# Optimization experiments

Measured on AMD Instinct MI355X. Metric: run time of the kernel, lower is better.

The kernel has to match this reference:

```python
import jax, jax.numpy as jnp
import numpy as np

B, INDIM, OUTDIM = 1024, 2048, 4096


def setup_inputs() -> dict:
    key = jax.random.key(0)
    kx, kw, kb = jax.random.split(key, 3)
    x = jax.random.normal(kx, (B, INDIM), dtype=jnp.float32)
    # nn.Linear(indim, outdim): weight [outdim, indim], bias [outdim]
    bound = 1.0 / np.sqrt(INDIM)
    W = jax.random.uniform(kw, (OUTDIM, INDIM), minval=-bound, maxval=bound, dtype=jnp.float32)
    b = jax.random.uniform(kb, (OUTDIM,), minval=-bound, maxval=bound, dtype=jnp.float32)
    return {"x": x, "W": W, "b": b}


def reference(x, W, b):
    # Faithful to torch: prototypes = weight.transpose(0,1).reshape(outdim, indim)
    # (a reflatten of W^T, not the original weight rows, since outdim != indim).
    protos = W.T.reshape(W.shape[0], W.shape[1])  # [outdim, indim]
    # -||x_i - p_j||^2 - b_j via GEMM identity (same math as broadcast subtract + norm^2)
    x_sq = jnp.sum(x * x, axis=1, keepdims=True)          # [B, 1]
    p_sq = jnp.sum(protos * protos, axis=1)[None, :]      # [1, outdim]
    xp = jnp.einsum('bd,od->bo', x, protos)               # [B, outdim]
    return -(x_sq - 2.0 * xp + p_sq) - b[None, :]
```

## Files before the change

### kernel.cpp

```cpp
#include <hip/hip_runtime.h>

#define IN_DIM  2048
#define OUT_DIM 4096

typedef float     f32x4 __attribute__((ext_vector_type(4)));
typedef long long llx2  __attribute__((ext_vector_type(2)));

__device__ __forceinline__ unsigned int pk4(float a, float b, float c, float d) {
    int v = __builtin_amdgcn_cvt_pk_fp8_f32(a, b, 0, false);
    v     = __builtin_amdgcn_cvt_pk_fp8_f32(c, d, v, true);
    return (unsigned int)v;
}

__device__ __forceinline__ void async16(const void* g, void* l) {
    __builtin_amdgcn_global_load_lds(
        (const __attribute__((address_space(1))) unsigned int*)g,
        (__attribute__((address_space(3))) unsigned int*)l,
        16, 0, 0);
}

__device__ __forceinline__ int gmem_of(int c) { return 2 * (c & 3) + (c >> 2); }

extern "C" __global__ __launch_bounds__(256) void prep(
        const float* __restrict__ W, const float* __restrict__ x,
        unsigned char* __restrict__ protos, unsigned char* __restrict__ xb,
        float* __restrict__ psq_part, float* __restrict__ x_sq) {
    __shared__ float tile[64][65];
    const int t = threadIdx.x;

    if (blockIdx.z == 2) {
        const int b = blockIdx.x + 32 * blockIdx.y;
        const float* xp = x + (size_t)b * IN_DIM + t * 8;
        const float4 v0 = ((const float4*)xp)[0];
        const float4 v1 = ((const float4*)xp)[1];
        uint2 pk;
        pk.x = pk4(v0.x, v0.y, v0.z, v0.w);
        pk.y = pk4(v1.x, v1.y, v1.z, v1.w);
        *(uint2*)(xb + (size_t)b * IN_DIM + (t >> 3) * 64 + gmem_of(t & 7) * 8) = pk;

        float s = v0.x * v0.x + v0.y * v0.y + v0.z * v0.z + v0.w * v0.w
                + v1.x * v1.x + v1.y * v1.y + v1.z * v1.z + v1.w * v1.w;
#pragma unroll
        for (int off = 32; off > 0; off >>= 1) s += __shfl_down(s, off);
        const int lane = t & 63, w = t >> 6;
        if (lane == 0) tile[0][w] = s;
        __syncthreads();
        if (t == 0) x_sq[b] = tile[0][0] + tile[0][1] + tile[0][2] + tile[0][3];
        return;
    }

    const int r  = blockIdx.z;
    const int c0 = blockIdx.x * 64;
    const int d0 = blockIdx.y * 64;
    const int g  = t >> 4;
    const int cc = (t & 15) * 4;

    const float* Wp = W + (size_t)(r * IN_DIM + d0 + g) * IN_DIM + c0 + cc;
#pragma unroll
    for (int p = 0; p < 4; ++p) {
        const float4 v = *(const float4*)(Wp + (size_t)(16 * p) * IN_DIM);
        const int dl = g + 16 * p;
        tile[dl][cc]     = v.x;
        tile[dl][cc + 1] = v.y;
        tile[dl][cc + 2] = v.z;
        tile[dl][cc + 3] = v.w;
    }
    __syncthreads();

    const int c8 = t & 7;
    const int gm = gmem_of(c8);
#pragma unroll
    for (int p = 0; p < 2; ++p) {
        const int cr = (t >> 3) + 32 * p;
        float v[8];
        float ss = 0.f;
#pragma unroll
        for (int j = 0; j < 8; ++j) {
            v[j] = tile[8 * c8 + j][cr];
            ss += v[j] * v[j];
        }
        const int o = 2 * (c0 + cr) + r;
        uint2 pk;
        pk.x = pk4(16.f * v[0], 16.f * v[1], 16.f * v[2], 16.f * v[3]);
        pk.y = pk4(16.f * v[4], 16.f * v[5], 16.f * v[6], 16.f * v[7]);
        *(uint2*)(protos + (size_t)o * IN_DIM + d0 + gm * 8) = pk;
        ss += __shfl_xor(ss, 1);
        ss += __shfl_xor(ss, 2);
        ss += __shfl_xor(ss, 4);
        if (c8 == 0) psq_part[(size_t)blockIdx.y * OUT_DIM + o] = ss;
    }
}

extern "C" __global__ __launch_bounds__(256, 4) void gemm_epi(
        const unsigned char* __restrict__ A,
        const unsigned char* __restrict__ Bt,
        const float* __restrict__ x_sq,
        const float* __restrict__ psq_part,
        const float* __restrict__ bias,
        float* __restrict__ out) {
    __shared__ __align__(16) unsigned char smem[16384];
    unsigned char* lA = smem;

    const int lid = blockIdx.x;
    const int xcd = lid & 7;
    const int wi  = lid >> 3;
    const int nt  = xcd * 8 + (wi & 7);
    const int mt  = wi >> 3;
    const int m0 = mt * 64;
    const int n0 = nt * 64;

    const int t = threadIdx.x;
    const int rS = t >> 3;
    const int pS = t & 7;
    const int lS = pS ^ (rS & 7);
    const size_t goff = (size_t)(lS >> 2) * 1024 + (lS & 3) * 16;
    const unsigned char* gA0 = A  + (size_t)(m0 + rS) * IN_DIM + goff;
    const unsigned char* gA1 = gA0 + (size_t)32 * IN_DIM;
    unsigned char* lAd = lA + t * 16;

    const int wave = t >> 6;
    const int lane = t & 63;
    const int kh = wave & 1;
    const int nh = wave >> 1;
    const int ln = lane & 15;
    const int qd = lane >> 4;
    const int pr = (kh * 4 + qd) ^ (ln & 7);

    const unsigned char* gBf = Bt + (size_t)(n0 + nh * 32 + ln) * IN_DIM
                                  + kh * 1024 + qd * 16;

    f32x4 acc[4][2] = {};

    for (int it = 0; it < 16; ++it) {
        async16(gA0, lAd); async16(gA1, lAd + 4096);
        gA0 += 64; gA1 += 64;
        llx2 bf[2];
        bf[0] = *(const llx2*)(gBf);
        bf[1] = *(const llx2*)(gBf + (size_t)16 * IN_DIM);
        gBf += 64;
        __syncthreads();

        llx2 af[4];
#pragma unroll
        for (int i = 0; i < 4; ++i)
            af[i] = *(const llx2*)(lA + (i * 16 + ln) * 128 + pr * 16);
#pragma unroll
        for (int kk = 0; kk < 2; ++kk)
#pragma unroll
            for (int i = 0; i < 4; ++i)
#pragma unroll
                for (int j = 0; j < 2; ++j)
                    acc[i][j] = __builtin_amdgcn_mfma_f32_16x16x32_fp8_fp8(
                                    af[i][kk], bf[j][kk], acc[i][j], 0, 0, 0);
        __syncthreads();
    }

    if (kh == 1) {
#pragma unroll
        for (int i = 0; i < 4; ++i)
#pragma unroll
            for (int j = 0; j < 2; ++j)
                *(f32x4*)(smem + nh * 8192 + (i * 2 + j) * 1024 + lane * 16) =
                    acc[i][j];
    }
    __syncthreads();
    if (kh == 0) {
#pragma unroll
        for (int j = 0; j < 2; ++j) {
            const int col = n0 + nh * 32 + j * 16 + ln;
            float pb = bias[col];
#pragma unroll
            for (int dt = 0; dt < 32; ++dt)
                pb += psq_part[(size_t)dt * OUT_DIM + col];
#pragma unroll
            for (int i = 0; i < 4; ++i) {
                const f32x4 o4 = *(const f32x4*)(smem + nh * 8192 +
                                                 (i * 2 + j) * 1024 + lane * 16);
                const int row0 = m0 + i * 16 + qd * 4;
#pragma unroll
                for (int rr = 0; rr < 4; ++rr) {
                    const int row = row0 + rr;
                    out[(size_t)row * OUT_DIM + col] =
                        0.125f * (acc[i][j][rr] + o4[rr]) - x_sq[row] - pb;
                }
            }
        }
    }
}

extern "C" void kernel_launch(void* const* d_in, const int* in_sizes, int n_in,
                              void* d_out, int out_size, void* d_ws, size_t ws_size,
                              hipStream_t stream) {
    const float* x    = (const float*)d_in[0];
    const float* W    = (const float*)d_in[1];
    const float* bias = (const float*)d_in[2];
    float* out = (float*)d_out;

    char* ws = (char*)d_ws;
    unsigned char* protos = (unsigned char*)ws;
    unsigned char* xb     = (unsigned char*)(ws + (size_t)8 * 1024 * 1024);
    float* x_sq           = (float*)(ws + (size_t)10 * 1024 * 1024);
    float* psq_part       = (float*)(ws + (size_t)10 * 1024 * 1024 + 65536);

    prep<<<dim3(32, 32, 3), 256, 0, stream>>>(W, x, protos, xb, psq_part, x_sq);
    gemm_epi<<<dim3(1024), 256, 0, stream>>>(xb, protos, x_sq, psq_part, bias, out);
}
```

Baseline: 115.2 us.

## Drop LDS staging and split-K; load GEMM operands directly from global memory

Removes the LDS staging of A tiles and the split-K across wave pairs. Each wave now reads its A and B fragments straight from global memory, with 64x128 tiles per block and 512 blocks, and there is no shared-memory reduction or barrier. This removes synchronization and the cross-wave reduction in the epilogue. In exchange, all four waves redundantly load the same A rows from global and cache, and the loop has a longer serial K. Memory latency is also no longer hidden by async LDS loads.

```diff
diff --git a/kernel.cpp b/kernel.cpp
--- a/kernel.cpp
+++ b/kernel.cpp
@@ -10,13 +10,6 @@
     int v = __builtin_amdgcn_cvt_pk_fp8_f32(a, b, 0, false);
     v     = __builtin_amdgcn_cvt_pk_fp8_f32(c, d, v, true);
     return (unsigned int)v;
-}
-
-__device__ __forceinline__ void async16(const void* g, void* l) {
-    __builtin_amdgcn_global_load_lds(
-        (const __attribute__((address_space(1))) unsigned int*)g,
-        (__attribute__((address_space(3))) unsigned int*)l,
-        16, 0, 0);
 }
 
 __device__ __forceinline__ int gmem_of(int c) { return 2 * (c & 3) + (c >> 2); }
@@ -91,59 +84,40 @@
     }
 }
 
-extern "C" __global__ __launch_bounds__(256, 4) void gemm_epi(
+extern "C" __global__ __launch_bounds__(256) void gemm_epi(
         const unsigned char* __restrict__ A,
         const unsigned char* __restrict__ Bt,
         const float* __restrict__ x_sq,
         const float* __restrict__ psq_part,
         const float* __restrict__ bias,
         float* __restrict__ out) {
-    __shared__ __align__(16) unsigned char smem[16384];
-    unsigned char* lA = smem;
-
     const int lid = blockIdx.x;
     const int xcd = lid & 7;
     const int wi  = lid >> 3;
-    const int nt  = xcd * 8 + (wi & 7);
-    const int mt  = wi >> 3;
+    const int nt  = xcd * 4 + (wi & 3);
+    const int mt  = wi >> 2;
     const int m0 = mt * 64;
-    const int n0 = nt * 64;
+    const int n0 = nt * 128;
 
     const int t = threadIdx.x;
-    const int rS = t >> 3;
-    const int pS = t & 7;
-    const int lS = pS ^ (rS & 7);
-    const size_t goff = (size_t)(lS >> 2) * 1024 + (lS & 3) * 16;
-    const unsigned char* gA0 = A  + (size_t)(m0 + rS) * IN_DIM + goff;
-    const unsigned char* gA1 = gA0 + (size_t)32 * IN_DIM;
-    unsigned char* lAd = lA + t * 16;
-
     const int wave = t >> 6;
     const int lane = t & 63;
-    const int kh = wave & 1;
-    const int nh = wave >> 1;
     const int ln = lane & 15;
     const int qd = lane >> 4;
-    const int pr = (kh * 4 + qd) ^ (ln & 7);
 
-    const unsigned char* gBf = Bt + (size_t)(n0 + nh * 32 + ln) * IN_DIM
-                                  + kh * 1024 + qd * 16;
+    const unsigned char* gA = A  + (size_t)(m0 + ln) * IN_DIM + qd * 16;
+    const unsigned char* gB = Bt + (size_t)(n0 + wave * 32 + ln) * IN_DIM + qd * 16;
 
     f32x4 acc[4][2] = {};
 
-    for (int it = 0; it < 16; ++it) {
-        async16(gA0, lAd); async16(gA1, lAd + 4096);
-        gA0 += 64; gA1 += 64;
-        llx2 bf[2];
-        bf[0] = *(const llx2*)(gBf);
-        bf[1] = *(const llx2*)(gBf + (size_t)16 * IN_DIM);
-        gBf += 64;
-        __syncthreads();
-
-        llx2 af[4];
+    for (int it = 0; it < 32; ++it) {
+        llx2 af[4], bf[2];
 #pragma unroll
         for (int i = 0; i < 4; ++i)
-            af[i] = *(const llx2*)(lA + (i * 16 + ln) * 128 + pr * 16);
+            af[i] = *(const llx2*)(gA + (size_t)(i * 16) * IN_DIM + it * 64);
+#pragma unroll
+        for (int j = 0; j < 2; ++j)
+            bf[j] = *(const llx2*)(gB + (size_t)(j * 16) * IN_DIM + it * 64);
 #pragma unroll
         for (int kk = 0; kk < 2; ++kk)
 #pragma unroll
@@ -152,37 +126,23 @@
                 for (int j = 0; j < 2; ++j)
                     acc[i][j] = __builtin_amdgcn_mfma_f32_16x16x32_fp8_fp8(
                                     af[i][kk], bf[j][kk], acc[i][j], 0, 0, 0);
-        __syncthreads();
     }
 
-    if (kh == 1) {
 #pragma unroll
-        for (int i = 0; i < 4; ++i)
+    for (int j = 0; j < 2; ++j) {
+        const int col = n0 + wave * 32 + j * 16 + ln;
+        float pb = bias[col];
 #pragma unroll
-            for (int j = 0; j < 2; ++j)
-                *(f32x4*)(smem + nh * 8192 + (i * 2 + j) * 1024 + lane * 16) =
-                    acc[i][j];
-    }
-    __syncthreads();
-    if (kh == 0) {
+        for (int dt = 0; dt < 32; ++dt)
+            pb += psq_part[(size_t)dt * OUT_DIM + col];
 #pragma unroll
-        for (int j = 0; j < 2; ++j) {
-            const int col = n0 + nh * 32 + j * 16 + ln;
-            float pb = bias[col];
+        for (int i = 0; i < 4; ++i) {
+            const int row0 = m0 + i * 16 + qd * 4;
 #pragma unroll
-            for (int dt = 0; dt < 32; ++dt)
-                pb += psq_part[(size_t)dt * OUT_DIM + col];
-#pragma unroll
-            for (int i = 0; i < 4; ++i) {
-                const f32x4 o4 = *(const f32x4*)(smem + nh * 8192 +
-                                                 (i * 2 + j) * 1024 + lane * 16);
-                const int row0 = m0 + i * 16 + qd * 4;
-#pragma unroll
-                for (int rr = 0; rr < 4; ++rr) {
-                    const int row = row0 + rr;
-                    out[(size_t)row * OUT_DIM + col] =
-                        0.125f * (acc[i][j][rr] + o4[rr]) - x_sq[row] - pb;
-                }
+            for (int rr = 0; rr < 4; ++rr) {
+                const int row = row0 + rr;
+                out[(size_t)row * OUT_DIM + col] =
+                    0.125f * acc[i][j][rr] - x_sq[row] - pb;
             }
         }
     }
@@ -203,5 +163,5 @@
     float* psq_part       = (float*)(ws + (size_t)10 * 1024 * 1024 + 65536);
 
     prep<<<dim3(32, 32, 3), 256, 0, stream>>>(W, x, protos, xb, psq_part, x_sq);
-    gemm_epi<<<dim3(1024), 256, 0, stream>>>(xb, protos, x_sq, psq_part, bias, out);
+    gemm_epi<<<dim3(512), 256, 0, stream>>>(xb, protos, x_sq, psq_part, bias, out);
 }
```

After: 141.4 us. 22.8% more time.
